# Optimization experiments

Hardware: AMD Instinct MI355X
Metric: run time of the kernel (lower is better)

## Reference

```python
import jax, jax.numpy as jnp
import numpy as np
from jax import lax

EPS = 1e-6
B, C, F, K = 64, 512, 1024, 3

def rmsnorm2d(x, w):
    # normalize over channel dim (axis=1), learnable per-channel scale
    inv = lax.rsqrt(jnp.mean(x * x, axis=1, keepdims=True) + EPS)
    return x * inv * w[None, :, None, None]

def pointwise(x, W, b):
    # 1x1 conv == per-pixel matmul: [B,C,H,F] x [O,C] -> [B,O,H,F]
    return jnp.einsum('bchf,oc->bohf', x, W) + b[None, :, None, None]

def depthwise_band(x, W, b):
    # depthwise conv, kernel (1,K), same padding along freq axis
    y = lax.conv_general_dilated(
        x, W,
        window_strides=(1, 1),
        padding=((0, 0), (K // 2, K // 2)),
        dimension_numbers=('NCHW', 'OIHW', 'NCHW'),
        feature_group_count=C)
    return y + b[None, :, None, None]

def setup_inputs() -> dict:
    key = jax.random.key(0)
    ks = jax.random.split(key, 6)
    s = 0.02
    return {
        'x_t': jax.random.normal(ks[0], (B, C, 1, F), jnp.float32),
        'h_prev': jax.random.normal(ks[1], (B, C, 1, F), jnp.float32),
        'in_norm_w': jnp.ones((C,), jnp.float32),
        'hid_norm_w': jnp.ones((C,), jnp.float32),
        'out_norm_w': jnp.ones((C,), jnp.float32),
        'xW': jax.random.normal(ks[2], (3 * C, C), jnp.float32) * s,
        'xb': jnp.zeros((3 * C,), jnp.float32),
        'hmixW': jax.random.normal(ks[3], (C, 1, 1, K), jnp.float32) * s,
        'hmixb': jnp.zeros((C,), jnp.float32),
        'hW': jax.random.normal(ks[4], (3 * C, C), jnp.float32) * s,
        'hb': jnp.zeros((3 * C,), jnp.float32),
    }

def reference(x_t, h_prev, in_norm_w, hid_norm_w, out_norm_w,
              xW, xb, hmixW, hmixb, hW, hb):
    xg = pointwise(rmsnorm2d(x_t, in_norm_w), xW, xb)            # [B,3C,1,F]
    hg = pointwise(depthwise_band(rmsnorm2d(h_prev, hid_norm_w), hmixW, hmixb), hW, hb)
    xr, xz, xn = jnp.split(xg, 3, axis=1)
    hr, hz, hn = jnp.split(hg, 3, axis=1)
    reset = jax.nn.sigmoid(xr + hr)
    update = jax.nn.sigmoid(xz + hz)
    cand = jnp.tanh(xn + reset * hn)
    h_new = (1.0 - update) * cand + update * h_prev
    return rmsnorm2d(h_new + x_t, out_norm_w)
```

## Files before the change

kernel.cpp:

```cpp
#include <hip/hip_runtime.h>

typedef __attribute__((ext_vector_type(8))) short short8;
typedef __attribute__((ext_vector_type(4))) float f32x4;
typedef __attribute__((ext_vector_type(4))) unsigned short u16x4;
typedef unsigned short u16;
typedef unsigned int u32;

#define EPSV 1e-6f

__device__ __forceinline__ u16 f2bf(float f){
  u32 u = __float_as_uint(f);
  u = u + 0x7fffu + ((u >> 16) & 1u);
  return (u16)(u >> 16);
}
__device__ __forceinline__ float bf2f(u16 h){
  return __uint_as_float(((u32)h) << 16);
}
__device__ __forceinline__ float sigm(float v){ return 1.f/(1.f + __expf(-v)); }
__device__ __forceinline__ float tanh_fast(float g){
  float e = __expf(-2.f*fabsf(g));
  return copysignf((1.f - e)/(1.f + e), g);
}
__device__ __forceinline__ void gload_lds16(const void* g, void* l){
  __builtin_amdgcn_global_load_lds(
      (const __attribute__((address_space(1))) u32*)g,
      (__attribute__((address_space(3))) u32*)l, 16, 0, 0);
}

#define WS_WXB   0u
#define WS_WHB   1572864u
#define WS_CB    3145728u
#define WS_SSQP  3153920u
#define WS_SBF   7348224u
#define WS_NEED  74457088u

#define GG_SMEM  132096

extern "C" __global__ void wprep(const float* __restrict__ xW, const float* __restrict__ hW,
                                 const float* __restrict__ inw, const float* __restrict__ hidw,
                                 const float* __restrict__ xb, const float* __restrict__ hmixb,
                                 const float* __restrict__ hb,
                                 u16* __restrict__ xWb, u16* __restrict__ hWb,
                                 float* __restrict__ cb){
  __shared__ float red[4];
  const int n = blockIdx.x;
  const int tid = threadIdx.x;
  float pb = 0.f;
  for (int k = tid; k < 512; k += 256){
    float xw = xW[n*512 + k], hw = hW[n*512 + k];
    xWb[n*512 + k] = f2bf(xw * inw[k]);
    hWb[n*512 + k] = f2bf(hw * hidw[k]);
    pb += hw * hmixb[k];
  }
  #pragma unroll
  for (int off = 1; off < 64; off <<= 1) pb += __shfl_xor(pb, off);
  if ((tid & 63) == 0) red[tid >> 6] = pb;
  __syncthreads();
  if (tid == 0){
    float dot = red[0] + red[1] + red[2] + red[3];
    if (n < 1024){ cb[n] = xb[n] + hb[n] + dot; }
    else         { cb[n] = xb[n]; cb[n + 512] = hb[n] + dot; }
  }
}

extern "C" __global__ void __launch_bounds__(256)
wbuild(const float* __restrict__ x, const float* __restrict__ h,
       const float* __restrict__ hmixW,
       u16* __restrict__ Ax, u16* __restrict__ Ahm)
{
  __shared__ float tile[32][264];
  __shared__ float invx_s[256];
  __shared__ float invh_s[258];
  __shared__ float hmw_s[1536];

  const int b = blockIdx.y, fc = blockIdx.x;
  const int f0 = fc*256;
  const int t = threadIdx.x;
  const int r = t >> 3, q = t & 7;

  for (int i = t; i < 1536; i += 256) hmw_s[i] = hmixW[i];

  float ssq = 0.f;
  for (int cc = 0; cc < 16; ++cc){
    __syncthreads();
    const float* src = x + ((size_t)(b*512 + cc*32 + r))*1024 + f0;
    #pragma unroll
    for (int i = 0; i < 8; ++i)
      *(f32x4*)&tile[r][q*4 + i*32] = *(const f32x4*)(src + q*4 + i*32);
    __syncthreads();
    float p = 0.f;
    #pragma unroll
    for (int rr = 0; rr < 32; ++rr){ float v = tile[rr][t]; p += v*v; }
    ssq += p;
  }
  invx_s[t] = rsqrtf(ssq*(1.f/512.f) + EPSV);
  for (int cc = 0; cc < 16; ++cc){
    __syncthreads();
    const float* src = x + ((size_t)(b*512 + cc*32 + r))*1024 + f0;
    #pragma unroll
    for (int i = 0; i < 8; ++i)
      *(f32x4*)&tile[r][q*4 + i*32] = *(const f32x4*)(src + q*4 + i*32);
    __syncthreads();
    #pragma unroll
    for (int it = 0; it < 4; ++it){
      int id = it*256 + t;
      int pix = id >> 2, c8 = (id & 3)*8;
      float iv = invx_s[pix];
      short8 pk;
      #pragma unroll
      for (int j = 0; j < 8; ++j) pk[j] = (short)f2bf(tile[c8+j][pix]*iv);
      *(short8*)(Ax + ((size_t)(b*1024 + f0 + pix))*512 + cc*32 + c8) = pk;
    }
  }
  float ssqh = 0.f, ssqL = 0.f, ssqR = 0.f;
  for (int cc = 0; cc < 16; ++cc){
    __syncthreads();
    const float* src = h + ((size_t)(b*512 + cc*32 + r))*1024 + f0;
    #pragma unroll
    for (int i = 0; i < 8; ++i)
      *(f32x4*)&tile[r][q*4 + i*32] = *(const f32x4*)(src + q*4 + i*32);
    if (t < 32){
      tile[t][256] = (f0 > 0) ? h[((size_t)(b*512 + cc*32 + t))*1024 + f0 - 1] : 0.f;
    } else if (t < 64){
      int rr = t - 32;
      tile[rr][257] = (f0 + 256 < 1024) ? h[((size_t)(b*512 + cc*32 + rr))*1024 + f0 + 256] : 0.f;
    }
    __syncthreads();
    float p = 0.f;
    #pragma unroll
    for (int rr = 0; rr < 32; ++rr){ float v = tile[rr][t]; p += v*v; }
    ssqh += p;
    if (t == 0){ float p2=0.f; for (int rr=0; rr<32; ++rr){ float v=tile[rr][256]; p2+=v*v; } ssqL += p2; }
    if (t == 1){ float p2=0.f; for (int rr=0; rr<32; ++rr){ float v=tile[rr][257]; p2+=v*v; } ssqR += p2; }
  }
  invh_s[1 + t] = rsqrtf(ssqh*(1.f/512.f) + EPSV);
  if (t == 0) invh_s[0]   = rsqrtf(ssqL*(1.f/512.f) + EPSV);
  if (t == 1) invh_s[257] = rsqrtf(ssqR*(1.f/512.f) + EPSV);
  for (int cc = 0; cc < 16; ++cc){
    __syncthreads();
    const float* src = h + ((size_t)(b*512 + cc*32 + r))*1024 + f0;
    #pragma unroll
    for (int i = 0; i < 8; ++i)
      *(f32x4*)&tile[r][q*4 + i*32] = *(const f32x4*)(src + q*4 + i*32);
    if (t < 32){
      tile[t][256] = (f0 > 0) ? h[((size_t)(b*512 + cc*32 + t))*1024 + f0 - 1] : 0.f;
    } else if (t < 64){
      int rr = t - 32;
      tile[rr][257] = (f0 + 256 < 1024) ? h[((size_t)(b*512 + cc*32 + rr))*1024 + f0 + 256] : 0.f;
    }
    __syncthreads();
    #pragma unroll
    for (int it = 0; it < 4; ++it){
      int id = it*256 + t;
      int pix = id >> 2, c8 = (id & 3)*8;
      int colL = (pix == 0)   ? 256 : (pix - 1);
      int colR = (pix == 255) ? 257 : (pix + 1);
      float iL = invh_s[pix], iC = invh_s[pix+1], iR = invh_s[pix+2];
      short8 pk;
      #pragma unroll
      for (int j = 0; j < 8; ++j){
        int c = c8 + j;
        int cg = cc*32 + c;
        float v = hmw_s[cg*3+0]*tile[c][colL]*iL
                + hmw_s[cg*3+1]*tile[c][pix ]*iC
                + hmw_s[cg*3+2]*tile[c][colR]*iR;
        pk[j] = (short)f2bf(v);
      }
      *(short8*)(Ahm + ((size_t)(b*1024 + f0 + pix))*512 + cc*32 + c8) = pk;
    }
  }
}

extern "C" __global__ void __launch_bounds__(512, 2)
gemm_gates(const float* __restrict__ x, const float* __restrict__ h,
           const u16* __restrict__ Abase,
           const u16* __restrict__ xWb, const u16* __restrict__ hWb,
           const float* __restrict__ cb,
           float* __restrict__ ssqp, u16* __restrict__ sbf)
{
  extern __shared__ __align__(16) char smem[];
  const int t = threadIdx.x;
  const int bid = blockIdx.x;
  const int swz = (bid & 7)*256 + (bid >> 3);
  const int mh = swz >> 4, ch = swz & 15;
  const int b = mh >> 1, f0 = (mh & 1)*512;
  const int c0 = ch*32;
  const int pixbase = b*1024 + f0;
  const int w = t >> 6, lane = t & 63, li = lane & 15, lg = lane >> 4;

  char* Bbase = smem;

  auto stageB = [&](const u16* Wsrc){
    #pragma unroll
    for (int i = 0; i < 12; ++i){
      int fi = i*8 + w;
      int kk = fi / 6, rem = fi - kk*6;
      int g = rem >> 1, ct = rem & 1;
      gload_lds16(Wsrc + ((size_t)(g*512 + c0 + ct*16 + li))*512 + kk*32 + lg*8,
                  Bbase + fi*1024);
    }
  };
  const size_t arow = ((size_t)(pixbase + w*64 + li))*512 + lg*8;
  auto loadA = [&](const u16* Asrc, int kk, short8 (&dst)[4]){
    #pragma unroll
    for (int mf = 0; mf < 4; ++mf)
      dst[mf] = *(const short8*)(Asrc + arow + (size_t)mf*16*512 + kk*32);
  };

  f32x4 accr[2][4] = {}, accz[2][4] = {}, accg1[2][4] = {}, accg2[2][4] = {};

  auto kstepR = [&](int kk, const short8 (&af)[4], f32x4 (&accg)[2][4]){
    #pragma unroll
    for (int ct = 0; ct < 2; ++ct){
      const char* bb = Bbase + (kk*6 + ct)*1024 + lane*16;
      short8 bf0 = *(const short8*)(bb);
      short8 bf1 = *(const short8*)(bb + 2048);
      short8 bf2 = *(const short8*)(bb + 4096);
      #pragma unroll
      for (int mf = 0; mf < 4; ++mf){
        accr[ct][mf] = __builtin_amdgcn_mfma_f32_16x16x32_bf16(af[mf], bf0, accr[ct][mf], 0,0,0);
        accz[ct][mf] = __builtin_amdgcn_mfma_f32_16x16x32_bf16(af[mf], bf1, accz[ct][mf], 0,0,0);
        accg[ct][mf] = __builtin_amdgcn_mfma_f32_16x16x32_bf16(af[mf], bf2, accg[ct][mf], 0,0,0);
      }
    }
  };

  short8 aE[4], aO[4];

  stageB(xWb);
  loadA(Abase, 0, aE);
  loadA(Abase, 1, aO);
  __syncthreads();
  #pragma unroll
  for (int jj = 0; jj < 8; ++jj){
    kstepR(2*jj, aE, accg1);
    if (jj < 7) loadA(Abase, 2*jj + 2, aE);
    kstepR(2*jj + 1, aO, accg1);
    if (jj < 7) loadA(Abase, 2*jj + 3, aO);
  }
  __syncthreads();
  const u16* A1 = Abase + 33554432;
  stageB(hWb);
  loadA(A1, 0, aE);
  loadA(A1, 1, aO);
  __syncthreads();
  #pragma unroll
  for (int jj = 0; jj < 8; ++jj){
    kstepR(2*jj, aE, accg2);
    if (jj < 7) loadA(A1, 2*jj + 2, aE);
    kstepR(2*jj + 1, aO, accg2);
    if (jj < 7) loadA(A1, 2*jj + 3, aO);
  }
  __syncthreads();

  float (*stgX)[516] = (float(*)[516])smem;
  float (*stgH)[516] = (float(*)[516])(smem + 66048);
  {
    const int col = (t & 127)*4;
    const int r0  = t >> 7;
    #pragma unroll
    for (int p2 = 0; p2 < 8; ++p2){
      int row = p2*4 + r0;
      const size_t g = ((size_t)(b*512 + c0 + row))*1024 + f0 + col;
      *(f32x4*)&stgX[row][col] = *(const f32x4*)(x + g);
      *(f32x4*)&stgH[row][col] = *(const f32x4*)(h + g);
    }
  }
  __syncthreads();

  float ps[4][4] = {};
  #pragma unroll
  for (int ct = 0; ct < 2; ++ct){
    const int c = c0 + ct*16 + li;
    const float cbr = cb[c], cbz = cb[512 + c], xbn = cb[1024 + c], hbn = cb[1536 + c];
    #pragma unroll
    for (int mf = 0; mf < 4; ++mf){
      const int fcol = w*64 + mf*16 + lg*4;
      f32x4 hp = *(const f32x4*)&stgH[ct*16 + li][fcol];
      f32x4 xt = *(const f32x4*)&stgX[ct*16 + li][fcol];
      f32x4 sv;
      #pragma unroll
      for (int j = 0; j < 4; ++j){
        float rr = sigm(accr[ct][mf][j] + cbr);
        float zz = sigm(accz[ct][mf][j] + cbz);
        float g  = accg1[ct][mf][j] + xbn + rr*(accg2[ct][mf][j] + hbn);
        float th = tanh_fast(g);
        float s  = (1.f - zz)*th + zz*hp[j] + xt[j];
        sv[j] = s;
        ps[mf][j] += s*s;
      }
      *(f32x4*)&stgX[ct*16 + li][fcol] = sv;
    }
  }
  #pragma unroll
  for (int off = 1; off < 16; off <<= 1)
    #pragma unroll
    for (int mf = 0; mf < 4; ++mf)
      #pragma unroll
      for (int j = 0; j < 4; ++j)
        ps[mf][j] += __shfl_xor(ps[mf][j], off);
  if (li == 0){
    #pragma unroll
    for (int mf = 0; mf < 4; ++mf){
      f32x4 v; v[0]=ps[mf][0]; v[1]=ps[mf][1]; v[2]=ps[mf][2]; v[3]=ps[mf][3];
      *(f32x4*)(ssqp + (size_t)ch*65536 + pixbase + w*64 + mf*16 + lg*4) = v;
    }
  }
  __syncthreads();
  {
    const int cl = t >> 4, seg = t & 15;
    u16* dst = sbf + ((size_t)(b*512 + c0 + cl))*1024 + f0 + seg*32;
    #pragma unroll
    for (int qq = 0; qq < 2; ++qq){
      f32x4 a0 = *(const f32x4*)&stgX[cl][seg*32 + qq*16 + 0];
      f32x4 a1 = *(const f32x4*)&stgX[cl][seg*32 + qq*16 + 4];
      f32x4 a2 = *(const f32x4*)&stgX[cl][seg*32 + qq*16 + 8];
      f32x4 a3 = *(const f32x4*)&stgX[cl][seg*32 + qq*16 + 12];
      short8 p0, p1;
      #pragma unroll
      for (int j = 0; j < 4; ++j){
        p0[j]   = (short)f2bf(a0[j]); p0[j+4] = (short)f2bf(a1[j]);
        p1[j]   = (short)f2bf(a2[j]); p1[j+4] = (short)f2bf(a3[j]);
      }
      *(short8*)(dst + qq*16)     = p0;
      *(short8*)(dst + qq*16 + 8) = p1;
    }
  }
}

extern "C" __global__ void __launch_bounds__(256)
outnorm(const float* __restrict__ ssqp, const u16* __restrict__ sbf,
        const float* __restrict__ outw, float* __restrict__ out)
{
  __shared__ float invf[1024];
  const int b = blockIdx.y, cch = blockIdx.x;
  const int t = threadIdx.x;
  f32x4 acc = {};
  #pragma unroll
  for (int p = 0; p < 16; ++p){
    f32x4 v = *(const f32x4*)(ssqp + (size_t)p*65536 + b*1024 + t*4);
    acc[0]+=v[0]; acc[1]+=v[1]; acc[2]+=v[2]; acc[3]+=v[3];
  }
  f32x4 iv;
  #pragma unroll
  for (int j = 0; j < 4; ++j) iv[j] = rsqrtf(acc[j]*(1.f/512.f) + EPSV);
  *(f32x4*)&invf[t*4] = iv;
  __syncthreads();
  for (int cl = 0; cl < 32; ++cl){
    const int c = cch*32 + cl;
    const float ow = outw[c];
    const u16* row = sbf + ((size_t)(b*512 + c))*1024;
    u16x4 sv = *(const u16x4*)(row + t*4);
    f32x4 o;
    #pragma unroll
    for (int j = 0; j < 4; ++j) o[j] = bf2f(sv[j]) * invf[t*4 + j] * ow;
    *(f32x4*)(out + ((size_t)(b*512 + c))*1024 + t*4) = o;
  }
}

#define FB_AXN_OFF 0
#define FB_AHM_OFF 32768
#define FB_RAW_OFF 65536
#define FB_PART_OFF 102400
#define FB_INVX_OFF 104512
#define FB_INVH_OFF 104640
#define FB_SSQ2_OFF 104784
#define FB_INVO_OFF 105936
#define FB_SMEM_BYTES 106112

extern "C" __global__ void fb_wconv(const float* __restrict__ xW, const float* __restrict__ hW,
                                    u16* __restrict__ xWb, u16* __restrict__ hWb){
  int i = blockIdx.x*256 + threadIdx.x;
  xWb[i] = f2bf(xW[i]);
  hWb[i] = f2bf(hW[i]);
}

extern "C" __global__ void __launch_bounds__(512, 2)
fb_gru(const float* __restrict__ x, const float* __restrict__ h,
       const float* __restrict__ inw, const float* __restrict__ hidw,
       const float* __restrict__ outw,
       const float* __restrict__ xb, const float* __restrict__ hmixWc,
       const float* __restrict__ hmixb, const float* __restrict__ hb,
       const u16* __restrict__ xWb, const u16* __restrict__ hWb,
       float* __restrict__ out)
{
  extern __shared__ __align__(16) char smem[];
  const int b  = blockIdx.y;
  const int f0 = blockIdx.x * 32;
  const int t  = threadIdx.x;
  u16* raw = (u16*)(smem + FB_RAW_OFF);
  float* part = (float*)(smem + FB_PART_OFF);
  {
    const int fq = t & 7, cb2 = t >> 3;
    #pragma unroll
    for (int pass = 0; pass < 8; ++pass){
      int c = pass*64 + cb2;
      f32x4 v = *(const f32x4*)(x + ((size_t)(b*512 + c))*1024 + f0 + fq*4);
      u16* d = raw + c*36 + fq*4;
      d[0] = f2bf(v[0]); d[1] = f2bf(v[1]); d[2] = f2bf(v[2]); d[3] = f2bf(v[3]);
    }
  }
  __syncthreads();
  {
    const int f = t & 31, cs = t >> 5;
    float p = 0.f;
    for (int i = 0; i < 32; ++i){ float v = bf2f(raw[(cs*32 + i)*36 + f]); p += v*v; }
    part[cs*33 + f] = p;
  }
  __syncthreads();
  if (t < 32){
    float s = 0.f;
    for (int i = 0; i < 16; ++i) s += part[i*33 + t];
    ((float*)(smem + FB_INVX_OFF))[t] = rsqrtf(s*(1.f/512.f) + EPSV);
  }
  __syncthreads();
  {
    const int f = t >> 4, cc = t & 15;
    const float iv = ((float*)(smem + FB_INVX_OFF))[f];
    #pragma unroll
    for (int it = 0; it < 4; ++it){
      int cbase = (cc + it*16)*8;
      short8 pk;
      #pragma unroll
      for (int j = 0; j < 8; ++j){
        float v = bf2f(raw[(cbase+j)*36 + f]) * iv * inw[cbase+j];
        pk[j] = (short)f2bf(v);
      }
      *(short8*)(smem + FB_AXN_OFF + f*1024 + ((cbase*2) ^ ((f&7)<<4))) = pk;
    }
  }
  __syncthreads();
  {
    const int fq = t & 7, cb2 = t >> 3;
    #pragma unroll
    for (int pass = 0; pass < 8; ++pass){
      int c = pass*64 + cb2;
      f32x4 v = *(const f32x4*)(h + ((size_t)(b*512 + c))*1024 + f0 + fq*4);
      u16* d = raw + c*36 + 1 + fq*4;
      d[0] = f2bf(v[0]); d[1] = f2bf(v[1]); d[2] = f2bf(v[2]); d[3] = f2bf(v[3]);
    }
    {
      int c = t;
      size_t base = ((size_t)(b*512 + c))*1024;
      float lv = (f0 > 0)          ? h[base + f0 - 1]  : 0.f;
      float rv = (f0 + 32 < 1024)  ? h[base + f0 + 32] : 0.f;
      raw[c*36 + 0]  = f2bf(lv);
      raw[c*36 + 33] = f2bf(rv);
    }
  }
  __syncthreads();
  {
    const int fw = t & 63, cs = t >> 6;
    if (fw < 34){
      float p = 0.f;
      for (int i = 0; i < 64; ++i){ float v = bf2f(raw[(cs*64 + i)*36 + fw]); p += v*v; }
      part[cs*35 + fw] = p;
    }
  }
  __syncthreads();
  if (t < 34){
    float s = 0.f;
    for (int i = 0; i < 8; ++i) s += part[i*35 + t];
    ((float*)(smem + FB_INVH_OFF))[t] = rsqrtf(s*(1.f/512.f) + EPSV);
  }
  __syncthreads();
  {
    const int fr = t >> 5, cc = t & 31;
    const float* invh = (const float*)(smem + FB_INVH_OFF);
    const float iL = invh[fr], iC = invh[fr + 1], iR = invh[fr + 2];
    #pragma unroll
    for (int it = 0; it < 2; ++it){
      const int cbase = (cc + it*32)*8;
      short8 o;
      #pragma unroll
      for (int j = 0; j < 8; ++j){
        int c = cbase + j;
        float hL = bf2f(raw[c*36 + fr])     * iL;
        float hC = bf2f(raw[c*36 + fr + 1]) * iC;
        float hR = bf2f(raw[c*36 + fr + 2]) * iR;
        float v = (hmixWc[c*3]*hL + hmixWc[c*3+1]*hC + hmixWc[c*3+2]*hR) * hidw[c] + hmixb[c];
        o[j] = (short)f2bf(v);
      }
      *(short8*)(smem + FB_AHM_OFF + fr*1024 + ((cbase*2) ^ ((fr&7)<<4))) = o;
    }
  }
  __syncthreads();
  const int wv = t >> 6, lane = t & 63, li = lane & 15, lg = lane >> 4;
  const int n0 = wv*64;
  f32x4 ar[2][4] = {}, az[2][4] = {}, axg[2][4] = {}, ahg[2][4] = {};
  #pragma unroll
  for (int src = 0; src < 2; ++src){
    const char* A = smem + (src ? FB_AHM_OFF : FB_AXN_OFF);
    const u16* W = src ? hWb : xWb;
    for (int k0 = 0; k0 < 512; k0 += 32){
      const int kb = (k0*2 + lg*16) ^ ((li & 7) << 4);
      short8 a0 = *(const short8*)(A + li*1024 + kb);
      short8 a1 = *(const short8*)(A + (li+16)*1024 + kb);
      #pragma unroll
      for (int nt = 0; nt < 4; ++nt){
        const u16* bp = W + (size_t)(n0 + nt*16 + li)*512 + k0 + lg*8;
        short8 br = *(const short8*)(bp);
        short8 bz = *(const short8*)(bp + 512*512);
        short8 bg = *(const short8*)(bp + 1024*512);
        ar[0][nt] = __builtin_amdgcn_mfma_f32_16x16x32_bf16(a0, br, ar[0][nt], 0,0,0);
        ar[1][nt] = __builtin_amdgcn_mfma_f32_16x16x32_bf16(a1, br, ar[1][nt], 0,0,0);
        az[0][nt] = __builtin_amdgcn_mfma_f32_16x16x32_bf16(a0, bz, az[0][nt], 0,0,0);
        az[1][nt] = __builtin_amdgcn_mfma_f32_16x16x32_bf16(a1, bz, az[1][nt], 0,0,0);
        if (src == 0){
          axg[0][nt] = __builtin_amdgcn_mfma_f32_16x16x32_bf16(a0, bg, axg[0][nt], 0,0,0);
          axg[1][nt] = __builtin_amdgcn_mfma_f32_16x16x32_bf16(a1, bg, axg[1][nt], 0,0,0);
        } else {
          ahg[0][nt] = __builtin_amdgcn_mfma_f32_16x16x32_bf16(a0, bg, ahg[0][nt], 0,0,0);
          ahg[1][nt] = __builtin_amdgcn_mfma_f32_16x16x32_bf16(a1, bg, ahg[1][nt], 0,0,0);
        }
      }
    }
  }
  float ps[8] = {0,0,0,0,0,0,0,0};
  #pragma unroll
  for (int nt = 0; nt < 4; ++nt){
    const int c = n0 + nt*16 + li;
    const float xbr = xb[c], xbz = xb[512+c], xbg = xb[1024+c];
    const float hbr = hb[c], hbz = hb[512+c], hbg = hb[1024+c];
    #pragma unroll
    for (int mt = 0; mt < 2; ++mt){
      const size_t idx = ((size_t)(b*512 + c))*1024 + f0 + mt*16 + lg*4;
      const f32x4 hp = *(const f32x4*)(h + idx);
      const f32x4 xt = *(const f32x4*)(x + idx);
      f32x4 sv;
      #pragma unroll
      for (int j = 0; j < 4; ++j){
        float rr = sigm(ar[mt][nt][j] + xbr + hbr);
        float zz = sigm(az[mt][nt][j] + xbz + hbz);
        float g  = axg[mt][nt][j] + xbg + rr*(ahg[mt][nt][j] + hbg);
        float th = tanh_fast(g);
        float hv = (1.f - zz)*th + zz*hp[j];
        float s  = hv + xt[j];
        sv[j] = s;
        ps[mt*4 + j] += s*s;
      }
      ar[mt][nt] = sv;
    }
  }
  #pragma unroll
  for (int off = 1; off < 16; off <<= 1){
    #pragma unroll
    for (int p = 0; p < 8; ++p) ps[p] += __shfl_xor(ps[p], off);
  }
  __syncthreads();
  float* stg = (float*)(smem + FB_AXN_OFF);
  #pragma unroll
  for (int nt = 0; nt < 4; ++nt){
    const int n = n0 + nt*16 + li;
    #pragma unroll
    for (int mt = 0; mt < 2; ++mt){
      const int m0 = mt*16 + lg*4;
      *(f32x4*)(stg + n*32 + (m0 ^ ((n & 7) << 2))) = ar[mt][nt];
    }
  }
  float* sq2 = (float*)(smem + FB_SSQ2_OFF);
  if (li == 0){
    #pragma unroll
    for (int p = 0; p < 8; ++p){
      int m = (p >> 2)*16 + lg*4 + (p & 3);
      sq2[m*9 + wv] = ps[p];
    }
  }
  __syncthreads();
  if (t < 32){
    float s = 0.f;
    for (int i = 0; i < 8; ++i) s += sq2[t*9 + i];
    ((float*)(smem + FB_INVO_OFF))[t] = rsqrtf(s*(1.f/512.f) + EPSV);
  }
  __syncthreads();
  {
    const float* invO = (const float*)(smem + FB_INVO_OFF);
    const int cb2 = t >> 3, chh = t & 7;
    #pragma unroll
    for (int pass = 0; pass < 8; ++pass){
      int c = pass*64 + cb2;
      int base = (chh*4) ^ ((c & 7) << 2);
      f32x4 v = *(const f32x4*)(stg + c*32 + base);
      float ow = outw[c];
      f32x4 o;
      #pragma unroll
      for (int j = 0; j < 4; ++j) o[j] = v[j] * invO[chh*4 + j] * ow;
      *(f32x4*)(out + ((size_t)(b*512 + c))*1024 + f0 + chh*4) = o;
    }
  }
}

extern "C" void kernel_launch(void* const* d_in, const int* in_sizes, int n_in,
                              void* d_out, int out_size, void* d_ws, size_t ws_size,
                              hipStream_t stream){
  (void)in_sizes; (void)n_in; (void)out_size;
  const float* x      = (const float*)d_in[0];
  const float* h      = (const float*)d_in[1];
  const float* inw    = (const float*)d_in[2];
  const float* hidw   = (const float*)d_in[3];
  const float* outw   = (const float*)d_in[4];
  const float* xW     = (const float*)d_in[5];
  const float* xb     = (const float*)d_in[6];
  const float* hmixW  = (const float*)d_in[7];
  const float* hmixb  = (const float*)d_in[8];
  const float* hW     = (const float*)d_in[9];
  const float* hb     = (const float*)d_in[10];

  if (ws_size >= (size_t)WS_NEED){
    u16*   xWb  = (u16*)((char*)d_ws + WS_WXB);
    u16*   hWb  = (u16*)((char*)d_ws + WS_WHB);
    float* cbw  = (float*)((char*)d_ws + WS_CB);
    float* ssqp = (float*)((char*)d_ws + WS_SSQP);
    u16*   sbf  = (u16*)((char*)d_ws + WS_SBF);
    u16*   Ax   = (u16*)d_out;

    hipFuncSetAttribute(reinterpret_cast<const void*>(gemm_gates),
                        hipFuncAttributeMaxDynamicSharedMemorySize, GG_SMEM);

    wprep<<<1536, 256, 0, stream>>>(xW, hW, inw, hidw, xb, hmixb, hb, xWb, hWb, cbw);
    wbuild<<<dim3(4, 64), 256, 0, stream>>>(x, h, hmixW, Ax, Ax + 33554432);
    gemm_gates<<<2048, 512, GG_SMEM, stream>>>(x, h, Ax, xWb, hWb, cbw, ssqp, sbf);
    outnorm<<<dim3(16, 64), 256, 0, stream>>>(ssqp, sbf, outw, (float*)d_out);
  } else {
    u16* xWb = (u16*)d_ws;
    u16* hWb = xWb + 786432;
    hipFuncSetAttribute(reinterpret_cast<const void*>(fb_gru),
                        hipFuncAttributeMaxDynamicSharedMemorySize, FB_SMEM_BYTES);
    fb_wconv<<<3072, 256, 0, stream>>>(xW, hW, xWb, hWb);
    dim3 grid(32, 64);
    fb_gru<<<grid, 512, FB_SMEM_BYTES, stream>>>(x, h, inw, hidw, outw,
                                                 xb, hmixW, hmixb, hb,
                                                 xWb, hWb, (float*)d_out);
  }
}
```

Baseline: 659.5 us.

## Halve gemm_gates channel tile to 16 and store partial sums as bf16

Each gemm_gates block now covers 16 output channels instead of 32. This halves the accumulator registers and shared memory, raises launch bounds to 4 blocks per CU and doubles the grid to 4096 blocks. The per-channel-group sum-of-squares partials are stored as bf16 in 32 partitions instead of fp32 in 16, and outnorm sums them. The goal is higher occupancy and better latency hiding. The cost is that every A tile is reloaded twice as often, with less reuse per block, and the bf16 partial sums lose precision in the normalization.

```diff
diff --git a/kernel.cpp b/kernel.cpp
--- a/kernel.cpp
+++ b/kernel.cpp
@@ -34,7 +34,7 @@
 #define WS_SBF   7348224u
 #define WS_NEED  74457088u
 
-#define GG_SMEM  132096
+#define GG_SMEM  66048
 
 extern "C" __global__ void wprep(const float* __restrict__ xW, const float* __restrict__ hW,
                                  const float* __restrict__ inw, const float* __restrict__ hidw,
@@ -171,20 +171,20 @@
   }
 }
 
-extern "C" __global__ void __launch_bounds__(512, 2)
+extern "C" __global__ void __launch_bounds__(512, 4)
 gemm_gates(const float* __restrict__ x, const float* __restrict__ h,
            const u16* __restrict__ Abase,
            const u16* __restrict__ xWb, const u16* __restrict__ hWb,
            const float* __restrict__ cb,
-           float* __restrict__ ssqp, u16* __restrict__ sbf)
+           u16* __restrict__ ssqp, u16* __restrict__ sbf)
 {
   extern __shared__ __align__(16) char smem[];
   const int t = threadIdx.x;
   const int bid = blockIdx.x;
-  const int swz = (bid & 7)*256 + (bid >> 3);
-  const int mh = swz >> 4, ch = swz & 15;
+  const int swz = (bid & 7)*512 + (bid >> 3);
+  const int mh = swz >> 5, ch = swz & 31;
   const int b = mh >> 1, f0 = (mh & 1)*512;
-  const int c0 = ch*32;
+  const int c0 = ch*16;
   const int pixbase = b*1024 + f0;
   const int w = t >> 6, lane = t & 63, li = lane & 15, lg = lane >> 4;
 
@@ -192,11 +192,10 @@
 
   auto stageB = [&](const u16* Wsrc){
     #pragma unroll
-    for (int i = 0; i < 12; ++i){
+    for (int i = 0; i < 6; ++i){
       int fi = i*8 + w;
-      int kk = fi / 6, rem = fi - kk*6;
-      int g = rem >> 1, ct = rem & 1;
-      gload_lds16(Wsrc + ((size_t)(g*512 + c0 + ct*16 + li))*512 + kk*32 + lg*8,
+      int kk = fi / 3, g = fi - kk*3;
+      gload_lds16(Wsrc + ((size_t)(g*512 + c0 + li))*512 + kk*32 + lg*8,
                   Bbase + fi*1024);
     }
   };
@@ -207,21 +206,18 @@
       dst[mf] = *(const short8*)(Asrc + arow + (size_t)mf*16*512 + kk*32);
   };
 
-  f32x4 accr[2][4] = {}, accz[2][4] = {}, accg1[2][4] = {}, accg2[2][4] = {};
-
-  auto kstepR = [&](int kk, const short8 (&af)[4], f32x4 (&accg)[2][4]){
-    #pragma unroll
-    for (int ct = 0; ct < 2; ++ct){
-      const char* bb = Bbase + (kk*6 + ct)*1024 + lane*16;
-      short8 bf0 = *(const short8*)(bb);
-      short8 bf1 = *(const short8*)(bb + 2048);
-      short8 bf2 = *(const short8*)(bb + 4096);
-      #pragma unroll
-      for (int mf = 0; mf < 4; ++mf){
-        accr[ct][mf] = __builtin_amdgcn_mfma_f32_16x16x32_bf16(af[mf], bf0, accr[ct][mf], 0,0,0);
-        accz[ct][mf] = __builtin_amdgcn_mfma_f32_16x16x32_bf16(af[mf], bf1, accz[ct][mf], 0,0,0);
-        accg[ct][mf] = __builtin_amdgcn_mfma_f32_16x16x32_bf16(af[mf], bf2, accg[ct][mf], 0,0,0);
-      }
+  f32x4 accr[4] = {}, accz[4] = {}, accg1[4] = {}, accg2[4] = {};
+
+  auto kstepR = [&](int kk, const short8 (&af)[4], f32x4 (&accg)[4]){
+    const char* bb = Bbase + (kk*3)*1024 + lane*16;
+    short8 bf0 = *(const short8*)(bb);
+    short8 bf1 = *(const short8*)(bb + 1024);
+    short8 bf2 = *(const short8*)(bb + 2048);
+    #pragma unroll
+    for (int mf = 0; mf < 4; ++mf){
+      accr[mf] = __builtin_amdgcn_mfma_f32_16x16x32_bf16(af[mf], bf0, accr[mf], 0,0,0);
+      accz[mf] = __builtin_amdgcn_mfma_f32_16x16x32_bf16(af[mf], bf1, accz[mf], 0,0,0);
+      accg[mf] = __builtin_amdgcn_mfma_f32_16x16x32_bf16(af[mf], bf2, accg[mf], 0,0,0);
     }
   };
 
@@ -254,12 +250,12 @@
   __syncthreads();
 
   float (*stgX)[516] = (float(*)[516])smem;
-  float (*stgH)[516] = (float(*)[516])(smem + 66048);
+  float (*stgH)[516] = (float(*)[516])(smem + 33024);
   {
     const int col = (t & 127)*4;
     const int r0  = t >> 7;
     #pragma unroll
-    for (int p2 = 0; p2 < 8; ++p2){
+    for (int p2 = 0; p2 < 4; ++p2){
       int row = p2*4 + r0;
       const size_t g = ((size_t)(b*512 + c0 + row))*1024 + f0 + col;
       *(f32x4*)&stgX[row][col] = *(const f32x4*)(x + g);
@@ -269,27 +265,26 @@
   __syncthreads();
 
   float ps[4][4] = {};
-  #pragma unroll
-  for (int ct = 0; ct < 2; ++ct){
-    const int c = c0 + ct*16 + li;
+  {
+    const int c = c0 + li;
     const float cbr = cb[c], cbz = cb[512 + c], xbn = cb[1024 + c], hbn = cb[1536 + c];
     #pragma unroll
     for (int mf = 0; mf < 4; ++mf){
       const int fcol = w*64 + mf*16 + lg*4;
-      f32x4 hp = *(const f32x4*)&stgH[ct*16 + li][fcol];
-      f32x4 xt = *(const f32x4*)&stgX[ct*16 + li][fcol];
+      f32x4 hp = *(const f32x4*)&stgH[li][fcol];
+      f32x4 xt = *(const f32x4*)&stgX[li][fcol];
       f32x4 sv;
       #pragma unroll
       for (int j = 0; j < 4; ++j){
-        float rr = sigm(accr[ct][mf][j] + cbr);
-        float zz = sigm(accz[ct][mf][j] + cbz);
-        float g  = accg1[ct][mf][j] + xbn + rr*(accg2[ct][mf][j] + hbn);
+        float rr = sigm(accr[mf][j] + cbr);
+        float zz = sigm(accz[mf][j] + cbz);
+        float g  = accg1[mf][j] + xbn + rr*(accg2[mf][j] + hbn);
         float th = tanh_fast(g);
         float s  = (1.f - zz)*th + zz*hp[j] + xt[j];
         sv[j] = s;
         ps[mf][j] += s*s;
       }
-      *(f32x4*)&stgX[ct*16 + li][fcol] = sv;
+      *(f32x4*)&stgX[li][fcol] = sv;
     }
   }
   #pragma unroll
@@ -302,34 +297,33 @@
   if (li == 0){
     #pragma unroll
     for (int mf = 0; mf < 4; ++mf){
-      f32x4 v; v[0]=ps[mf][0]; v[1]=ps[mf][1]; v[2]=ps[mf][2]; v[3]=ps[mf][3];
-      *(f32x4*)(ssqp + (size_t)ch*65536 + pixbase + w*64 + mf*16 + lg*4) = v;
-    }
-  }
-  __syncthreads();
-  {
-    const int cl = t >> 4, seg = t & 15;
-    u16* dst = sbf + ((size_t)(b*512 + c0 + cl))*1024 + f0 + seg*32;
-    #pragma unroll
-    for (int qq = 0; qq < 2; ++qq){
-      f32x4 a0 = *(const f32x4*)&stgX[cl][seg*32 + qq*16 + 0];
-      f32x4 a1 = *(const f32x4*)&stgX[cl][seg*32 + qq*16 + 4];
-      f32x4 a2 = *(const f32x4*)&stgX[cl][seg*32 + qq*16 + 8];
-      f32x4 a3 = *(const f32x4*)&stgX[cl][seg*32 + qq*16 + 12];
-      short8 p0, p1;
-      #pragma unroll
-      for (int j = 0; j < 4; ++j){
-        p0[j]   = (short)f2bf(a0[j]); p0[j+4] = (short)f2bf(a1[j]);
-        p1[j]   = (short)f2bf(a2[j]); p1[j+4] = (short)f2bf(a3[j]);
-      }
-      *(short8*)(dst + qq*16)     = p0;
-      *(short8*)(dst + qq*16 + 8) = p1;
-    }
+      u16x4 v;
+      #pragma unroll
+      for (int j = 0; j < 4; ++j) v[j] = f2bf(ps[mf][j]);
+      *(u16x4*)(ssqp + (size_t)ch*65536 + pixbase + w*64 + mf*16 + lg*4) = v;
+    }
+  }
+  __syncthreads();
+  {
+    const int cl = t >> 5, seg = t & 31;
+    u16* dst = sbf + ((size_t)(b*512 + c0 + cl))*1024 + f0 + seg*16;
+    f32x4 a0 = *(const f32x4*)&stgX[cl][seg*16 + 0];
+    f32x4 a1 = *(const f32x4*)&stgX[cl][seg*16 + 4];
+    f32x4 a2 = *(const f32x4*)&stgX[cl][seg*16 + 8];
+    f32x4 a3 = *(const f32x4*)&stgX[cl][seg*16 + 12];
+    short8 p0, p1;
+    #pragma unroll
+    for (int j = 0; j < 4; ++j){
+      p0[j]   = (short)f2bf(a0[j]); p0[j+4] = (short)f2bf(a1[j]);
+      p1[j]   = (short)f2bf(a2[j]); p1[j+4] = (short)f2bf(a3[j]);
+    }
+    *(short8*)(dst)     = p0;
+    *(short8*)(dst + 8) = p1;
   }
 }
 
 extern "C" __global__ void __launch_bounds__(256)
-outnorm(const float* __restrict__ ssqp, const u16* __restrict__ sbf,
+outnorm(const u16* __restrict__ ssqp, const u16* __restrict__ sbf,
         const float* __restrict__ outw, float* __restrict__ out)
 {
   __shared__ float invf[1024];
@@ -337,9 +331,9 @@
   const int t = threadIdx.x;
   f32x4 acc = {};
   #pragma unroll
-  for (int p = 0; p < 16; ++p){
-    f32x4 v = *(const f32x4*)(ssqp + (size_t)p*65536 + b*1024 + t*4);
-    acc[0]+=v[0]; acc[1]+=v[1]; acc[2]+=v[2]; acc[3]+=v[3];
+  for (int p = 0; p < 32; ++p){
+    u16x4 v = *(const u16x4*)(ssqp + (size_t)p*65536 + b*1024 + t*4);
+    acc[0]+=bf2f(v[0]); acc[1]+=bf2f(v[1]); acc[2]+=bf2f(v[2]); acc[3]+=bf2f(v[3]);
   }
   f32x4 iv;
   #pragma unroll
@@ -610,7 +604,7 @@
     u16*   xWb  = (u16*)((char*)d_ws + WS_WXB);
     u16*   hWb  = (u16*)((char*)d_ws + WS_WHB);
     float* cbw  = (float*)((char*)d_ws + WS_CB);
-    float* ssqp = (float*)((char*)d_ws + WS_SSQP);
+    u16*   ssqp = (u16*)((char*)d_ws + WS_SSQP);
     u16*   sbf  = (u16*)((char*)d_ws + WS_SBF);
     u16*   Ax   = (u16*)d_out;
 
@@ -619,7 +613,7 @@
 
     wprep<<<1536, 256, 0, stream>>>(xW, hW, inw, hidw, xb, hmixb, hb, xWb, hWb, cbw);
     wbuild<<<dim3(4, 64), 256, 0, stream>>>(x, h, hmixW, Ax, Ax + 33554432);
-    gemm_gates<<<2048, 512, GG_SMEM, stream>>>(x, h, Ax, xWb, hWb, cbw, ssqp, sbf);
+    gemm_gates<<<4096, 512, GG_SMEM, stream>>>(x, h, Ax, xWb, hWb, cbw, ssqp, sbf);
     outnorm<<<dim3(16, 64), 256, 0, stream>>>(ssqp, sbf, outw, (float*)d_out);
   } else {
     u16* xWb = (u16*)d_ws;
```

Result: slower. 781.0 us (+18.4%).
